# Kernel tuning notes

Hardware: AMD Instinct MI355X
Metric: run time of the kernel (lower is better)

Reference implementation:

```python
import jax, jax.numpy as jnp
import numpy as np

V, PV, D, H, NC = 100000, 50, 128, 128, 2
L, B = 512, 64


def setup_inputs() -> dict:
    key = jax.random.key(0)
    ks = jax.random.split(key, 20)
    s = 0.05
    x = jax.random.randint(ks[0], (L, B), 0, V)
    y = jax.random.randint(ks[1], (B,), 0, 2)
    p = jax.random.randint(ks[2], (L, B), 0, PV)
    # pack_padded_sequence requires descending lengths
    lengths = jnp.sort(jax.random.randint(ks[3], (B,), 1, L + 1))[::-1]
    idx = jnp.arange(L, dtype=jnp.int32)
    left_child = jnp.broadcast_to(idx - 1, (B, L))  # left-deep chain; -1 => no child
    right_child = jnp.full((B, L), -1, dtype=jnp.int32)
    return dict(
        x=x, y=y, p=p, lengths=lengths,
        left_child=left_child, right_child=right_child,
        embed=jax.random.normal(ks[4], (V, D)) * s,
        Wih_f=jax.random.normal(ks[5], (4 * H, D)) * s,
        Whh_f=jax.random.normal(ks[6], (4 * H, H)) * s,
        b_f=jnp.zeros((4 * H,)),
        Wih_b=jax.random.normal(ks[7], (4 * H, D)) * s,
        Whh_b=jax.random.normal(ks[8], (4 * H, H)) * s,
        b_b=jnp.zeros((4 * H,)),
        Wiou=jax.random.normal(ks[9], (D, 3 * H)) * s,
        Uiou=jax.random.normal(ks[10], (H, 3 * H)) * s,
        biou=jnp.zeros((3 * H,)),
        Wf=jax.random.normal(ks[11], (D, H)) * s,
        Uf=jax.random.normal(ks[12], (H, H)) * s,
        bf=jnp.zeros((H,)),
        Wout=jax.random.normal(ks[13], (NC, 2 * H)) * s,
        bout=jnp.zeros((NC,)),
        w1=jnp.ones(()),
        w2=jnp.ones(()),
    )


def _lstm_dir(emb, mask, Wih, Whh, b, reverse):
    # length-masked uni-directional LSTM (emulates packed sequence); PyTorch gate order i,f,g,o
    Bm = emb.shape[1]
    def step(carry, inp):
        h, c = carry
        xt, m = inp  # [B,D], [B,1]
        g = xt @ Wih.T + h @ Whh.T + b
        i, f, gg, o = jnp.split(g, 4, axis=-1)
        cn = jax.nn.sigmoid(f) * c + jax.nn.sigmoid(i) * jnp.tanh(gg)
        hn = jax.nn.sigmoid(o) * jnp.tanh(cn)
        return (jnp.where(m, hn, h), jnp.where(m, cn, c)), None
    init = (jnp.zeros((Bm, H), emb.dtype), jnp.zeros((Bm, H), emb.dtype))
    (hT, _cT), _ = jax.lax.scan(step, init, (emb, mask), reverse=reverse)
    return hT  # final hidden [B,H]


def _tree_lstm(emb_k, length, left, right, Wiou, Uiou, biou, Wf, Uf, bf):
    # child-sum binary tree LSTM over one sample; nodes in topological order
    x_iou = emb_k @ Wiou + biou  # [L,3H]
    x_f = emb_k @ Wf + bf        # [L,H]
    def step(carry, inp):
        h_all, c_all = carry
        j, li, ri = inp
        def child(ix):
            v = (ix >= 0).astype(emb_k.dtype)
            ixc = jnp.maximum(ix, 0)
            return h_all[ixc] * v, c_all[ixc] * v
        hl, cl = child(li)
        hr, cr = child(ri)
        iou = x_iou[j] + (hl + hr) @ Uiou
        i, o, u = jnp.split(iou, 3)
        fl = jax.nn.sigmoid(x_f[j] + hl @ Uf)
        fr = jax.nn.sigmoid(x_f[j] + hr @ Uf)
        c = jax.nn.sigmoid(i) * jnp.tanh(u) + fl * cl + fr * cr
        h = jax.nn.sigmoid(o) * jnp.tanh(c)
        return (h_all.at[j].set(h), c_all.at[j].set(c)), None
    init = (jnp.zeros((L, H), emb_k.dtype), jnp.zeros((L, H), emb_k.dtype))
    (h_all, c_all), _ = jax.lax.scan(
        step, init, (jnp.arange(L, dtype=jnp.int32), left, right))
    root = length - 1  # last valid node is the root of the chain
    return c_all[root], h_all[root]


def reference(x, y, p, lengths, left_child, right_child, embed,
              Wih_f, Whh_f, b_f, Wih_b, Whh_b, b_b,
              Wiou, Uiou, biou, Wf, Uf, bf, Wout, bout, w1, w2):
    emb = embed[x]  # [L,B,D]; dropout layers treated as identity (eval)
    mask = (jnp.arange(L)[:, None] < lengths[None, :])[:, :, None]
    sent_vec = _lstm_dir(emb, mask, Wih_f, Whh_f, b_f, False)  # hidden[0][0], [B,H]
    _hb = _lstm_dir(emb, mask, Wih_b, Whh_b, b_b, True)        # bwd dir (unused downstream)
    emb_b = jnp.transpose(emb, (1, 0, 2))  # [B,L,D]
    t_state, t_hidden = jax.vmap(
        lambda e, ln, l, r: _tree_lstm(e, ln, l, r, Wiou, Uiou, biou, Wf, Uf, bf)
    )(emb_b, lengths, left_child, right_child)  # [B,H] each
    t_hidden = w1 * t_hidden + w2 * sent_vec    # learned mix of tree root hidden & sentence vec
    tree_out = jnp.concatenate([t_state, t_hidden], axis=1)  # [B,2H]
    pred = jax.nn.sigmoid(tree_out @ Wout.T + bout)           # [B,2]
    true = jax.nn.one_hot(jnp.clip(y, 0, 1), NC, dtype=pred.dtype)
    pc = jnp.clip(pred, 1e-7, 1.0 - 1e-7)
    loss = -jnp.mean(true * jnp.log(pc) + (1.0 - true) * jnp.log(1.0 - pc))
    return loss
```

## Files before the change

### kernel.cpp

```cpp
#include <hip/hip_runtime.h>

typedef unsigned short u16;
typedef __attribute__((ext_vector_type(8))) short bf16x8;
typedef __attribute__((ext_vector_type(4))) float f32x4;

#define LSEQ 512
#define BN   64
#define DD   128
#define HH   128
#define CHUNK 64


__device__ __forceinline__ u16 f2b(float f) {
  union { float f; unsigned i; } v; v.f = f;
  unsigned i = v.i;
  return (u16)((i + 0x7fffu + ((i >> 16) & 1u)) >> 16);
}
__device__ __forceinline__ float rcpf(float x) {
  return __builtin_amdgcn_rcpf(x);
}
__device__ __forceinline__ float sigm(float x) {
  return rcpf(1.f + __expf(-x));
}
__device__ __forceinline__ float tanh_f(float x) {
  x = fminf(15.f, fmaxf(-15.f, x));
  float e = __expf(2.f * x);
  return (e - 1.f) * rcpf(e + 1.f);
}
__device__ __forceinline__ float clampg(float x, float hi) {
  return fmaxf(-hi, fminf(hi, x));
}

__global__ __launch_bounds__(512, 1) void chains_kernel(
    const int* __restrict__ x, const int* __restrict__ lengths,
    const float* __restrict__ embed,
    const float* __restrict__ Wih_f, const float* __restrict__ Whh_f,
    const float* __restrict__ b_f,
    const float* __restrict__ Wiou, const float* __restrict__ Uiou,
    const float* __restrict__ biou,
    const float* __restrict__ Wf, const float* __restrict__ Uf,
    const float* __restrict__ bfv,
    float* __restrict__ sent_vec, float* __restrict__ t_state,
    float* __restrict__ t_hidden) {
  const bool tree = blockIdx.x >= BN;
  const int b = blockIdx.x & (BN - 1);
  int len = lengths[b];
  len = (len < 1) ? 1 : (len > LSEQ ? LSEQ : len);
  const int tid = threadIdx.x;
  const int w = tid >> 6, l = tid & 63, lr = l & 15, lq = l >> 4;
  const int d = w * 16 + lr;

  __shared__ __align__(16) u16 echunk[CHUNK * 128];
  __shared__ __align__(16) float estage[8 * 16 * 16 * 4];
  __shared__ __align__(16) u16 aK[2][128];
  __shared__ int toks[LSEQ];

  bf16x8 bfragH[4][4], bfragE[4][4];
  if (!tree) {
#pragma unroll
    for (int g = 0; g < 4; g++) {
      const int n = g * 128 + w * 16 + lr;
#pragma unroll
      for (int ks = 0; ks < 4; ks++) {
        const int k0 = ks * 32 + lq * 8;
        {
          float4 lo = *(const float4*)(Whh_f + n * 128 + k0);
          float4 hi = *(const float4*)(Whh_f + n * 128 + k0 + 4);
          bf16x8 fr;
          fr[0] = (short)f2b(lo.x); fr[1] = (short)f2b(lo.y);
          fr[2] = (short)f2b(lo.z); fr[3] = (short)f2b(lo.w);
          fr[4] = (short)f2b(hi.x); fr[5] = (short)f2b(hi.y);
          fr[6] = (short)f2b(hi.z); fr[7] = (short)f2b(hi.w);
          bfragH[g][ks] = fr;
        }
        {
          float4 lo = *(const float4*)(Wih_f + n * 128 + k0);
          float4 hi = *(const float4*)(Wih_f + n * 128 + k0 + 4);
          bf16x8 fr;
          fr[0] = (short)f2b(lo.x); fr[1] = (short)f2b(lo.y);
          fr[2] = (short)f2b(lo.z); fr[3] = (short)f2b(lo.w);
          fr[4] = (short)f2b(hi.x); fr[5] = (short)f2b(hi.y);
          fr[6] = (short)f2b(hi.z); fr[7] = (short)f2b(hi.w);
          bfragE[g][ks] = fr;
        }
      }
    }
  } else {
#pragma unroll
    for (int g = 0; g < 4; g++) {
      const int col = (g < 3) ? (g * 128 + w * 16 + lr) : (w * 16 + lr);
#pragma unroll
      for (int ks = 0; ks < 4; ks++) {
        const int k0 = ks * 32 + lq * 8;
        bf16x8 fh, fe;
#pragma unroll
        for (int j = 0; j < 8; j++) {
          const int k = k0 + j;
          float vh, ve;
          if (g < 3) { vh = Uiou[k * 384 + col]; ve = Wiou[k * 384 + col]; }
          else       { vh = Uf[k * 128 + col];   ve = Wf[k * 128 + col]; }
          fh[j] = (short)f2b(vh);
          fe[j] = (short)f2b(ve);
        }
        bfragH[g][ks] = fh;
        bfragE[g][ks] = fe;
      }
    }
  }

  float bias0, bias1, bias2, bias3;
  if (!tree) {
    bias0 = b_f[d];        bias1 = b_f[128 + d];
    bias2 = b_f[256 + d];  bias3 = b_f[384 + d];
  } else {
    bias0 = biou[d];       bias1 = biou[128 + d];
    bias2 = biou[256 + d]; bias3 = bfv[d];
  }

  for (int i = tid; i < LSEQ; i += 512) {
    int tt = (i < len) ? i : (len - 1);
    toks[i] = x[tt * BN + b];
  }
  if (tid < HH) { aK[0][tid] = 0; aK[1][tid] = 0; }

  char* const es_base = (char*)estage;
  const int erd = (w << 12) + (lr << 4);
  const int ewr = (w << 12) + (lq << 10) + (lr << 4);
  const char* const ak_rd = (const char*)aK + (lq << 4);
  u16* const ak_wr = &aK[0][0] + d;

  const f32x4 zf = (f32x4){0.f, 0.f, 0.f, 0.f};
  float c = 0.f, h = 0.f;
  int t = 0;

#define EBATCH(T0)                                                            \
  {                                                                           \
    const int rb = ((T0) & (CHUNK - 1)) + lr;                                 \
    bf16x8 ae[4];                                                             \
    _Pragma("unroll")                                                         \
    for (int ks = 0; ks < 4; ks++) {                                          \
      int bo = (rb * 256 + ks * 64 + lq * 16) ^ ((rb & 7) << 4);              \
      ae[ks] = *(const bf16x8*)((const char*)echunk + bo);                    \
    }                                                                         \
    f32x4 EBv[4];                                                             \
    _Pragma("unroll")                                                         \
    for (int g = 0; g < 4; g++)                                               \
      EBv[g] = __builtin_amdgcn_mfma_f32_16x16x32_bf16(ae[0], bfragE[g][0],   \
                                                       zf, 0, 0, 0);          \
    _Pragma("unroll")                                                         \
    for (int ks = 1; ks < 4; ks++)                                            \
      _Pragma("unroll")                                                       \
      for (int g = 0; g < 4; g++)                                             \
        EBv[g] = __builtin_amdgcn_mfma_f32_16x16x32_bf16(                     \
            ae[ks], bfragE[g][ks], EBv[g], 0, 0, 0);                          \
    _Pragma("unroll")                                                         \
    for (int rg = 0; rg < 4; rg++) {                                          \
      f32x4 wv = {EBv[0][rg], EBv[1][rg], EBv[2][rg], EBv[3][rg]};            \
      *(f32x4*)(es_base + ewr + rg * 256) = wv;                               \
    }                                                                         \
  }

#define STEPB(S)                                                              \
  {                                                                           \
    bf16x8 ah[4];                                                             \
    _Pragma("unroll")                                                         \
    for (int ks = 0; ks < 4; ks++)                                            \
      ah[ks] = *(const bf16x8*)(ak_rd + ((S) & 1) * 256 + ks * 64);           \
    f32x4 ev = *(const f32x4*)(es_base + erd + (S) * 256);                    \
    f32x4 acch[4];                                                            \
    _Pragma("unroll")                                                         \
    for (int g = 0; g < 4; g++)                                               \
      acch[g] = __builtin_amdgcn_mfma_f32_16x16x32_bf16(ah[0], bfragH[g][0],  \
                                                        zf, 0, 0, 0);         \
    _Pragma("unroll")                                                         \
    for (int ks = 1; ks < 4; ks++)                                            \
      _Pragma("unroll")                                                       \
      for (int g = 0; g < 4; g++)                                             \
        acch[g] = __builtin_amdgcn_mfma_f32_16x16x32_bf16(                    \
            ah[ks], bfragH[g][ks], acch[g], 0, 0, 0);                         \
    float g0 = clampg(acch[0][0] + ev[0] + bias0, 16.f);                      \
    float g1 = clampg(acch[1][0] + ev[1] + bias1, 16.f);                      \
    float g2 = clampg(acch[2][0] + ev[2] + bias2, 16.f);                      \
    float g3 = clampg(acch[3][0] + ev[3] + bias3, 16.f);                      \
    if (!tree) {                                                              \
      float ii = sigm(g0), ff = sigm(g1), gg = tanh_f(g2), oo = sigm(g3);     \
      c = ff * c + ii * gg;                                                   \
      h = oo * tanh_f(c);                                                     \
    } else {                                                                  \
      float ii = sigm(g0), oo = sigm(g1), uu = tanh_f(g2), fl = sigm(g3);     \
      c = ii * uu + fl * c;                                                   \
      h = oo * tanh_f(c);                                                     \
    }                                                                         \
    if (l < 16) ak_wr[(((S) & 1) ^ 1) * 128] = f2b(h);                        \
    __syncthreads();                                                          \
  }

#define STEPT(S) if (tb + (S) < tend) STEPB(S)

  for (int c0 = 0; c0 < len; c0 += CHUNK) {
    __syncthreads();

#pragma unroll
    for (int j = 0; j < 4; j++) {
      int u = tid + j * 512;
      int r = u >> 5;
      int c4 = (u & 31) * 4;
      int row = toks[c0 + r];
      float4 v = *(const float4*)(embed + (size_t)row * DD + c4);
      u16 eb[4] = {f2b(v.x), f2b(v.y), f2b(v.z), f2b(v.w)};
      int bo = (r * 256 + c4 * 2) ^ ((r & 7) << 4);
      *(unsigned long long*)((char*)echunk + bo) =
          *(const unsigned long long*)eb;
    }
    __syncthreads();

    const int tend = (c0 + CHUNK < len) ? c0 + CHUNK : len;
    while (t + 16 <= tend) {
      EBATCH(t)
      STEPB(0)  STEPB(1)  STEPB(2)  STEPB(3)
      STEPB(4)  STEPB(5)  STEPB(6)  STEPB(7)
      STEPB(8)  STEPB(9)  STEPB(10) STEPB(11)
      STEPB(12) STEPB(13) STEPB(14) STEPB(15)
      t += 16;
    }
    if (t < tend) {
      const int tb = t;
      EBATCH(tb)
      STEPT(0)  STEPT(1)  STEPT(2)  STEPT(3)
      STEPT(4)  STEPT(5)  STEPT(6)  STEPT(7)
      STEPT(8)  STEPT(9)  STEPT(10) STEPT(11)
      STEPT(12) STEPT(13) STEPT(14)
      t = tend;
    }
  }
#undef STEPT
#undef STEPB
#undef EBATCH

  if (l < 16) {
    if (!tree) {
      sent_vec[b * HH + d] = h;
    } else {
      t_state[b * HH + d] = c;
      t_hidden[b * HH + d] = h;
    }
  }
}

__global__ __launch_bounds__(128) void final_kernel(
    const int* __restrict__ y, const float* __restrict__ sent_vec,
    const float* __restrict__ t_state, const float* __restrict__ t_hidden,
    const float* __restrict__ Wout, const float* __restrict__ bout,
    const float* __restrict__ w1, const float* __restrict__ w2,
    float* __restrict__ out) {
  int tid = threadIdx.x;
  int b = tid >> 1, cls = tid & 1;
  float W1 = w1[0], W2 = w2[0];
  const float* wrow = Wout + cls * 256;
  float acc = bout[cls];
  for (int j = 0; j < HH; j++)
    acc += t_state[b * HH + j] * wrow[j];
  for (int j = 0; j < HH; j++)
    acc += (W1 * t_hidden[b * HH + j] + W2 * sent_vec[b * HH + j]) * wrow[128 + j];
  float p = 1.f / (1.f + __expf(-acc));
  p = fminf(1.f - 1e-7f, fmaxf(1e-7f, p));
  int yy = y[b]; yy = yy < 0 ? 0 : (yy > 1 ? 1 : yy);
  float term = (cls == yy) ? __logf(p) : __logf(1.f - p);
  __shared__ float red[128];
  red[tid] = term;
  __syncthreads();
  for (int s = 64; s > 0; s >>= 1) {
    if (tid < s) red[tid] += red[tid + s];
    __syncthreads();
  }
  if (tid == 0) out[0] = -red[0] / 128.f;
}

extern "C" void kernel_launch(void* const* d_in, const int* in_sizes, int n_in,
                              void* d_out, int out_size, void* d_ws, size_t ws_size,
                              hipStream_t stream) {
  (void)in_sizes; (void)n_in; (void)out_size; (void)ws_size;
  const int*   x       = (const int*)d_in[0];
  const int*   y       = (const int*)d_in[1];
  const int*   lengths = (const int*)d_in[3];
  const float* embed   = (const float*)d_in[6];
  const float* Wih_f   = (const float*)d_in[7];
  const float* Whh_f   = (const float*)d_in[8];
  const float* b_f     = (const float*)d_in[9];
  const float* Wiou    = (const float*)d_in[13];
  const float* Uiou    = (const float*)d_in[14];
  const float* biou    = (const float*)d_in[15];
  const float* Wf      = (const float*)d_in[16];
  const float* Uf      = (const float*)d_in[17];
  const float* bfv     = (const float*)d_in[18];
  const float* Wout    = (const float*)d_in[19];
  const float* bout    = (const float*)d_in[20];
  const float* w1      = (const float*)d_in[21];
  const float* w2      = (const float*)d_in[22];

  float* sent_vec = (float*)d_ws;
  float* t_state  = sent_vec + BN * HH;
  float* t_hidden = t_state + BN * HH;

  chains_kernel<<<128, 512, 0, stream>>>(x, lengths, embed,
                                         Wih_f, Whh_f, b_f,
                                         Wiou, Uiou, biou, Wf, Uf, bfv,
                                         sent_vec, t_state, t_hidden);
  final_kernel<<<1, 128, 0, stream>>>(y, sent_vec, t_state, t_hidden,
                                      Wout, bout, w1, w2, (float*)d_out);
}
```

Baseline: 392.8 us.

## Halve block to four waves, each computing 32 hidden units per step

Shrinks the recurrent LSTM block from 8 to 4 wavefronts. Each wave now owns two 16-column slices of the hidden state, so its weight fragments, gate accumulators, bias values and cell states are doubled, and the embedding stage buffer is re-laid out accordingly. The aim is to cut the cost of the per-timestep block barrier by having fewer waves to synchronise. In exchange, each wave issues twice as many MFMAs and nonlinearities per step on the serial critical path, and register pressure roughly doubles.

```diff
diff --git a/kernel.cpp b/kernel.cpp
--- a/kernel.cpp
+++ b/kernel.cpp
@@ -31,7 +31,7 @@
   return fmaxf(-hi, fminf(hi, x));
 }
 
-__global__ __launch_bounds__(512, 1) void chains_kernel(
+__global__ __launch_bounds__(256, 1) void chains_kernel(
     const int* __restrict__ x, const int* __restrict__ lengths,
     const float* __restrict__ embed,
     const float* __restrict__ Wih_f, const float* __restrict__ Whh_f,
@@ -48,89 +48,99 @@
   len = (len < 1) ? 1 : (len > LSEQ ? LSEQ : len);
   const int tid = threadIdx.x;
   const int w = tid >> 6, l = tid & 63, lr = l & 15, lq = l >> 4;
-  const int d = w * 16 + lr;
+  const int d0 = w * 32 + lr;
 
   __shared__ __align__(16) u16 echunk[CHUNK * 128];
-  __shared__ __align__(16) float estage[8 * 16 * 16 * 4];
+  __shared__ __align__(16) float estage[4 * 16 * 16 * 12];
   __shared__ __align__(16) u16 aK[2][128];
   __shared__ int toks[LSEQ];
 
-  bf16x8 bfragH[4][4], bfragE[4][4];
+  bf16x8 bfragH[4][2][4], bfragE[4][2][4];
   if (!tree) {
 #pragma unroll
-    for (int g = 0; g < 4; g++) {
-      const int n = g * 128 + w * 16 + lr;
-#pragma unroll
-      for (int ks = 0; ks < 4; ks++) {
-        const int k0 = ks * 32 + lq * 8;
-        {
-          float4 lo = *(const float4*)(Whh_f + n * 128 + k0);
-          float4 hi = *(const float4*)(Whh_f + n * 128 + k0 + 4);
-          bf16x8 fr;
-          fr[0] = (short)f2b(lo.x); fr[1] = (short)f2b(lo.y);
-          fr[2] = (short)f2b(lo.z); fr[3] = (short)f2b(lo.w);
-          fr[4] = (short)f2b(hi.x); fr[5] = (short)f2b(hi.y);
-          fr[6] = (short)f2b(hi.z); fr[7] = (short)f2b(hi.w);
-          bfragH[g][ks] = fr;
-        }
-        {
-          float4 lo = *(const float4*)(Wih_f + n * 128 + k0);
-          float4 hi = *(const float4*)(Wih_f + n * 128 + k0 + 4);
-          bf16x8 fr;
-          fr[0] = (short)f2b(lo.x); fr[1] = (short)f2b(lo.y);
-          fr[2] = (short)f2b(lo.z); fr[3] = (short)f2b(lo.w);
-          fr[4] = (short)f2b(hi.x); fr[5] = (short)f2b(hi.y);
-          fr[6] = (short)f2b(hi.z); fr[7] = (short)f2b(hi.w);
-          bfragE[g][ks] = fr;
+    for (int g = 0; g < 4; g++)
+#pragma unroll
+      for (int hh = 0; hh < 2; hh++) {
+        const int n = g * 128 + w * 32 + hh * 16 + lr;
+#pragma unroll
+        for (int ks = 0; ks < 4; ks++) {
+          const int k0 = ks * 32 + lq * 8;
+          {
+            float4 lo = *(const float4*)(Whh_f + n * 128 + k0);
+            float4 hi = *(const float4*)(Whh_f + n * 128 + k0 + 4);
+            bf16x8 fr;
+            fr[0] = (short)f2b(lo.x); fr[1] = (short)f2b(lo.y);
+            fr[2] = (short)f2b(lo.z); fr[3] = (short)f2b(lo.w);
+            fr[4] = (short)f2b(hi.x); fr[5] = (short)f2b(hi.y);
+            fr[6] = (short)f2b(hi.z); fr[7] = (short)f2b(hi.w);
+            bfragH[g][hh][ks] = fr;
+          }
+          {
+            float4 lo = *(const float4*)(Wih_f + n * 128 + k0);
+            float4 hi = *(const float4*)(Wih_f + n * 128 + k0 + 4);
+            bf16x8 fr;
+            fr[0] = (short)f2b(lo.x); fr[1] = (short)f2b(lo.y);
+            fr[2] = (short)f2b(lo.z); fr[3] = (short)f2b(lo.w);
+            fr[4] = (short)f2b(hi.x); fr[5] = (short)f2b(hi.y);
+            fr[6] = (short)f2b(hi.z); fr[7] = (short)f2b(hi.w);
+            bfragE[g][hh][ks] = fr;
+          }
         }
       }
-    }
   } else {
 #pragma unroll
-    for (int g = 0; g < 4; g++) {
-      const int col = (g < 3) ? (g * 128 + w * 16 + lr) : (w * 16 + lr);
-#pragma unroll
-      for (int ks = 0; ks < 4; ks++) {
-        const int k0 = ks * 32 + lq * 8;
-        bf16x8 fh, fe;
-#pragma unroll
-        for (int j = 0; j < 8; j++) {
-          const int k = k0 + j;
-          float vh, ve;
-          if (g < 3) { vh = Uiou[k * 384 + col]; ve = Wiou[k * 384 + col]; }
-          else       { vh = Uf[k * 128 + col];   ve = Wf[k * 128 + col]; }
-          fh[j] = (short)f2b(vh);
-          fe[j] = (short)f2b(ve);
+    for (int g = 0; g < 4; g++)
+#pragma unroll
+      for (int hh = 0; hh < 2; hh++) {
+        const int dcol = w * 32 + hh * 16 + lr;
+#pragma unroll
+        for (int ks = 0; ks < 4; ks++) {
+          const int k0 = ks * 32 + lq * 8;
+          bf16x8 fh, fe;
+#pragma unroll
+          for (int j = 0; j < 8; j++) {
+            const int k = k0 + j;
+            float vh, ve;
+            if (g < 3) { vh = Uiou[k * 384 + g * 128 + dcol];
+                         ve = Wiou[k * 384 + g * 128 + dcol]; }
+            else       { vh = Uf[k * 128 + dcol];
+                         ve = Wf[k * 128 + dcol]; }
+            fh[j] = (short)f2b(vh);
+            fe[j] = (short)f2b(ve);
+          }
+          bfragH[g][hh][ks] = fh;
+          bfragE[g][hh][ks] = fe;
         }
-        bfragH[g][ks] = fh;
-        bfragE[g][ks] = fe;
       }
-    }
-  }
-
-  float bias0, bias1, bias2, bias3;
+  }
+
+  float bA0, bA1, bA2, bA3, bB0, bB1, bB2, bB3;
   if (!tree) {
-    bias0 = b_f[d];        bias1 = b_f[128 + d];
-    bias2 = b_f[256 + d];  bias3 = b_f[384 + d];
+    bA0 = b_f[d0];        bA1 = b_f[128 + d0];
+    bA2 = b_f[256 + d0];  bA3 = b_f[384 + d0];
+    bB0 = b_f[d0 + 16];       bB1 = b_f[128 + d0 + 16];
+    bB2 = b_f[256 + d0 + 16]; bB3 = b_f[384 + d0 + 16];
   } else {
-    bias0 = biou[d];       bias1 = biou[128 + d];
-    bias2 = biou[256 + d]; bias3 = bfv[d];
-  }
-
-  for (int i = tid; i < LSEQ; i += 512) {
+    bA0 = biou[d0];       bA1 = biou[128 + d0];
+    bA2 = biou[256 + d0]; bA3 = bfv[d0];
+    bB0 = biou[d0 + 16];       bB1 = biou[128 + d0 + 16];
+    bB2 = biou[256 + d0 + 16]; bB3 = bfv[d0 + 16];
+  }
+
+  for (int i = tid; i < LSEQ; i += 256) {
     int tt = (i < len) ? i : (len - 1);
     toks[i] = x[tt * BN + b];
   }
   if (tid < HH) { aK[0][tid] = 0; aK[1][tid] = 0; }
 
   char* const es_base = (char*)estage;
-  const int erd = (w << 12) + (lr << 4);
-  const int ewr = (w << 12) + (lq << 10) + (lr << 4);
+  const int erd = w * 12288 + lr * 48;
+  const int ewr = w * 12288 + lq * 3072 + lr * 48;
   const char* const ak_rd = (const char*)aK + (lq << 4);
-  u16* const ak_wr = &aK[0][0] + d;
+  u16* const ak_wr = &aK[0][w * 32 + (l & 31)];
 
   const f32x4 zf = (f32x4){0.f, 0.f, 0.f, 0.f};
-  float c = 0.f, h = 0.f;
+  float c0 = 0.f, h0 = 0.f, c1 = 0.f, h1 = 0.f;
   int t = 0;
 
 #define EBATCH(T0)                                                            \
@@ -142,21 +152,27 @@
       int bo = (rb * 256 + ks * 64 + lq * 16) ^ ((rb & 7) << 4);              \
       ae[ks] = *(const bf16x8*)((const char*)echunk + bo);                    \
     }                                                                         \
-    f32x4 EBv[4];                                                             \
+    f32x4 EBv[4][2];                                                          \
     _Pragma("unroll")                                                         \
     for (int g = 0; g < 4; g++)                                               \
-      EBv[g] = __builtin_amdgcn_mfma_f32_16x16x32_bf16(ae[0], bfragE[g][0],   \
-                                                       zf, 0, 0, 0);          \
+      _Pragma("unroll")                                                       \
+      for (int hh = 0; hh < 2; hh++)                                          \
+        EBv[g][hh] = __builtin_amdgcn_mfma_f32_16x16x32_bf16(                 \
+            ae[0], bfragE[g][hh][0], zf, 0, 0, 0);                            \
     _Pragma("unroll")                                                         \
     for (int ks = 1; ks < 4; ks++)                                            \
       _Pragma("unroll")                                                       \
       for (int g = 0; g < 4; g++)                                             \
-        EBv[g] = __builtin_amdgcn_mfma_f32_16x16x32_bf16(                     \
-            ae[ks], bfragE[g][ks], EBv[g], 0, 0, 0);                          \
+        _Pragma("unroll")                                                     \
+        for (int hh = 0; hh < 2; hh++)                                        \
+          EBv[g][hh] = __builtin_amdgcn_mfma_f32_16x16x32_bf16(               \
+              ae[ks], bfragE[g][hh][ks], EBv[g][hh], 0, 0, 0);                \
     _Pragma("unroll")                                                         \
     for (int rg = 0; rg < 4; rg++) {                                          \
-      f32x4 wv = {EBv[0][rg], EBv[1][rg], EBv[2][rg], EBv[3][rg]};            \
-      *(f32x4*)(es_base + ewr + rg * 256) = wv;                               \
+      f32x4 w0 = {EBv[0][0][rg], EBv[1][0][rg], EBv[2][0][rg], EBv[3][0][rg]};\
+      f32x4 w1 = {EBv[0][1][rg], EBv[1][1][rg], EBv[2][1][rg], EBv[3][1][rg]};\
+      *(f32x4*)(es_base + ewr + rg * 768) = w0;                               \
+      *(f32x4*)(es_base + ewr + rg * 768 + 16) = w1;                          \
     }                                                                         \
   }
 
@@ -166,46 +182,58 @@
     _Pragma("unroll")                                                         \
     for (int ks = 0; ks < 4; ks++)                                            \
       ah[ks] = *(const bf16x8*)(ak_rd + ((S) & 1) * 256 + ks * 64);           \
-    f32x4 ev = *(const f32x4*)(es_base + erd + (S) * 256);                    \
-    f32x4 acch[4];                                                            \
+    f32x4 ev0 = *(const f32x4*)(es_base + erd + (S) * 768);                   \
+    f32x4 ev1 = *(const f32x4*)(es_base + erd + (S) * 768 + 16);              \
+    f32x4 acch[4][2];                                                         \
     _Pragma("unroll")                                                         \
     for (int g = 0; g < 4; g++)                                               \
-      acch[g] = __builtin_amdgcn_mfma_f32_16x16x32_bf16(ah[0], bfragH[g][0],  \
-                                                        zf, 0, 0, 0);         \
+      _Pragma("unroll")                                                       \
+      for (int hh = 0; hh < 2; hh++)                                          \
+        acch[g][hh] = __builtin_amdgcn_mfma_f32_16x16x32_bf16(                \
+            ah[0], bfragH[g][hh][0], zf, 0, 0, 0);                            \
     _Pragma("unroll")                                                         \
     for (int ks = 1; ks < 4; ks++)                                            \
       _Pragma("unroll")                                                       \
       for (int g = 0; g < 4; g++)                                             \
-        acch[g] = __builtin_amdgcn_mfma_f32_16x16x32_bf16(                    \
-            ah[ks], bfragH[g][ks], acch[g], 0, 0, 0);                         \
-    float g0 = clampg(acch[0][0] + ev[0] + bias0, 16.f);                      \
-    float g1 = clampg(acch[1][0] + ev[1] + bias1, 16.f);                      \
-    float g2 = clampg(acch[2][0] + ev[2] + bias2, 16.f);                      \
-    float g3 = clampg(acch[3][0] + ev[3] + bias3, 16.f);                      \
+        _Pragma("unroll")                                                     \
+        for (int hh = 0; hh < 2; hh++)                                        \
+          acch[g][hh] = __builtin_amdgcn_mfma_f32_16x16x32_bf16(              \
+              ah[ks], bfragH[g][hh][ks], acch[g][hh], 0, 0, 0);               \
+    float gA0 = clampg(acch[0][0][0] + ev0[0] + bA0, 16.f);                   \
+    float gA1 = clampg(acch[1][0][0] + ev0[1] + bA1, 16.f);                   \
+    float gA2 = clampg(acch[2][0][0] + ev0[2] + bA2, 16.f);                   \
+    float gA3 = clampg(acch[3][0][0] + ev0[3] + bA3, 16.f);                   \
+    float gB0 = clampg(acch[0][1][0] + ev1[0] + bB0, 16.f);                   \
+    float gB1 = clampg(acch[1][1][0] + ev1[1] + bB1, 16.f);                   \
+    float gB2 = clampg(acch[2][1][0] + ev1[2] + bB2, 16.f);                   \
+    float gB3 = clampg(acch[3][1][0] + ev1[3] + bB3, 16.f);                   \
     if (!tree) {                                                              \
-      float ii = sigm(g0), ff = sigm(g1), gg = tanh_f(g2), oo = sigm(g3);     \
-      c = ff * c + ii * gg;                                                   \
-      h = oo * tanh_f(c);                                                     \
+      float iA = sigm(gA0), fA = sigm(gA1), gA = tanh_f(gA2), oA = sigm(gA3); \
+      c0 = fA * c0 + iA * gA;  h0 = oA * tanh_f(c0);                          \
+      float iB = sigm(gB0), fB = sigm(gB1), gB = tanh_f(gB2), oB = sigm(gB3); \
+      c1 = fB * c1 + iB * gB;  h1 = oB * tanh_f(c1);                          \
     } else {                                                                  \
-      float ii = sigm(g0), oo = sigm(g1), uu = tanh_f(g2), fl = sigm(g3);     \
-      c = ii * uu + fl * c;                                                   \
-      h = oo * tanh_f(c);                                                     \
+      float iA = sigm(gA0), oA = sigm(gA1), uA = tanh_f(gA2), fA = sigm(gA3); \
+      c0 = iA * uA + fA * c0;  h0 = oA * tanh_f(c0);                          \
+      float iB = sigm(gB0), oB = sigm(gB1), uB = tanh_f(gB2), fB = sigm(gB3); \
+      c1 = iB * uB + fB * c1;  h1 = oB * tanh_f(c1);                          \
     }                                                                         \
-    if (l < 16) ak_wr[(((S) & 1) ^ 1) * 128] = f2b(h);                        \
+    float hsel = (l < 16) ? h0 : h1;                                          \
+    if (l < 32) ak_wr[(((S) & 1) ^ 1) * 128] = f2b(hsel);                     \
     __syncthreads();                                                          \
   }
 
 #define STEPT(S) if (tb + (S) < tend) STEPB(S)
 
-  for (int c0 = 0; c0 < len; c0 += CHUNK) {
+  for (int c0i = 0; c0i < len; c0i += CHUNK) {
     __syncthreads();
 
 #pragma unroll
-    for (int j = 0; j < 4; j++) {
-      int u = tid + j * 512;
+    for (int j = 0; j < 8; j++) {
+      int u = tid + j * 256;
       int r = u >> 5;
       int c4 = (u & 31) * 4;
-      int row = toks[c0 + r];
+      int row = toks[c0i + r];
       float4 v = *(const float4*)(embed + (size_t)row * DD + c4);
       u16 eb[4] = {f2b(v.x), f2b(v.y), f2b(v.z), f2b(v.w)};
       int bo = (r * 256 + c4 * 2) ^ ((r & 7) << 4);
@@ -214,7 +242,7 @@
     }
     __syncthreads();
 
-    const int tend = (c0 + CHUNK < len) ? c0 + CHUNK : len;
+    const int tend = (c0i + CHUNK < len) ? c0i + CHUNK : len;
     while (t + 16 <= tend) {
       EBATCH(t)
       STEPB(0)  STEPB(1)  STEPB(2)  STEPB(3)
@@ -237,12 +265,13 @@
 #undef STEPB
 #undef EBATCH
 
-  if (l < 16) {
+  if (l < 32) {
+    const int dd = w * 32 + l;
     if (!tree) {
-      sent_vec[b * HH + d] = h;
+      sent_vec[b * HH + dd] = (l < 16) ? h0 : h1;
     } else {
-      t_state[b * HH + d] = c;
-      t_hidden[b * HH + d] = h;
+      t_state[b * HH + dd] = (l < 16) ? c0 : c1;
+      t_hidden[b * HH + dd] = (l < 16) ? h0 : h1;
     }
   }
 }
@@ -302,7 +331,7 @@
   float* t_state  = sent_vec + BN * HH;
   float* t_hidden = t_state + BN * HH;
 
-  chains_kernel<<<128, 512, 0, stream>>>(x, lengths, embed,
+  chains_kernel<<<128, 256, 0, stream>>>(x, lengths, embed,
                                          Wih_f, Whh_f, b_f,
                                          Wiou, Uiou, biou, Wf, Uf, bfv,
                                          sent_vec, t_state, t_hidden);
```

Result: slower. 508.9 us (+29.6%).
